# Kernel optimization log

Hardware: AMD Instinct MI355X
Metric: run time of the kernel (lower is better)

Reference implementation:

```python
import jax, jax.numpy as jnp
import numpy as np

B = 32; N = 512; SEQ_LEN = 8
L = 0.05; T_REF = 5.0; V_TH = 20.0; V_RES = 0.0
SQL = float(np.sqrt(L))
BN_EPS = 1e-5

# ---- Dawson-style lookup tables for the LIF moment activation (built once, float64) ----
_XG = np.linspace(-10.0, 4.0, 7001)
_DX = _XG[1] - _XG[0]

def _cumtrapz(y):
    return np.concatenate([[0.0], np.cumsum(0.5 * (y[1:] + y[:-1]) * _DX)])

_phi = np.exp(-_XG ** 2)
_I = np.exp(-100.0) / 20.0 + _cumtrapz(_phi)          # int_{-inf}^x e^{-t^2} dt (asymptotic tail at -10)
_g = np.exp(_XG ** 2) * _I                             # 1st Dawson-like function g(x)
_G = _cumtrapz(_g)                                     # int g dx (rel. to -10)
_h = np.exp(_XG ** 2) * _cumtrapz(_phi * _g ** 2)      # 2nd Dawson-like function h(x)
_H = _cumtrapz(_h)                                     # int h dx

XG = jnp.asarray(_XG, jnp.float32)
GT = jnp.asarray(_g, jnp.float32)
GI = jnp.asarray(_G, jnp.float32)
HI = jnp.asarray(_H, jnp.float32)

def _interp(x, tab):
    return jnp.interp(x, XG, tab)

def moment_activate(u, s, rho):
    # Mnn_Activate_Mean / Std / Corr: LIF moment activation
    s = jnp.maximum(s, 1e-6)
    ub = jnp.clip((V_TH * L - u) / (s * SQL), -10.0, 4.0)
    lb = jnp.clip((V_RES * L - u) / (s * SQL), -10.0, 4.0)
    dG = _interp(ub, GI) - _interp(lb, GI)
    ua = 1.0 / (T_REF + (2.0 / L) * dG)                               # mean firing rate
    dH = jnp.maximum(_interp(ub, HI) - _interp(lb, HI), 0.0)
    sa = jnp.sqrt((8.0 / L ** 2) * dH * ua ** 3)                      # firing std
    dg = _interp(ub, GT) - _interp(lb, GT)
    chi = ua ** 2 * (2.0 / L) * dg / (SQL * jnp.maximum(sa, 1e-9))    # linear response coeff
    eye = jnp.eye(rho.shape[-1], dtype=rho.dtype)
    rho_out = chi[:, :, None] * chi[:, None, :] * rho                 # [B,N,N]
    rho_out = rho_out * (1.0 - eye) + eye                             # unit diagonal
    return ua, sa, rho_out

def linear_corr(W, b, u, s, rho):
    # Mnn_Linear_Corr: mean via affine map, covariance via W C W^T
    u_out = u @ W.T + b
    Cin = rho * s[:, :, None] * s[:, None, :]                         # [B,N,N] covariance
    C = jnp.einsum('bik,lk->bil', jnp.einsum('ij,bjk->bik', W, Cin), W)
    var = jnp.clip(jnp.diagonal(C, axis1=1, axis2=2), 0.0, None)
    s_out = jnp.sqrt(var)
    denom = s_out[:, :, None] * s_out[:, None, :]
    rho_out = jnp.where(denom > 1e-12, C / jnp.maximum(denom, 1e-12), 0.0)
    return u_out, s_out, rho_out

def mexi_hat(n, k=0.3):
    dx = 2.0 * np.pi / n
    x = np.arange(0.0, 2.0 * np.pi, dx)[:n]
    y = np.exp(2.0 * (np.cos(x) - 1.0)) * np.cos(2.0 * x)
    j = np.arange(n)
    idx = (j[None, :] - j[:, None]) % n                               # w[i,:] = y.roll(i)
    return y[idx].astype(np.float32)

def setup_inputs() -> dict:
    ks = jax.random.split(jax.random.key(0), 10)
    u = jax.random.normal(ks[0], (B, N), jnp.float32)
    s = jax.random.uniform(ks[1], (B, N), jnp.float32, 0.1, 1.0)
    A = jax.random.normal(ks[2], (B, N, N), jnp.float32) / np.sqrt(N)
    sym = 0.5 * (A + jnp.swapaxes(A, 1, 2))
    eye = jnp.eye(N, dtype=jnp.float32)
    rho = jnp.clip(sym, -0.5, 0.5) * (1.0 - eye) + eye                # valid-ish corr matrix
    u_ext = jax.random.normal(ks[3], (B, N), jnp.float32)
    s_ext = jax.random.uniform(ks[4], (B, N), jnp.float32, 0.1, 1.0)
    W = 0.02 * jax.random.normal(ks[5], (N, N), jnp.float32) + 0.1 * jnp.asarray(mexi_hat(N))
    b = 0.02 * jax.random.normal(ks[6], (N,), jnp.float32)
    W_ext = 0.02 * jax.random.normal(ks[7], (N, N), jnp.float32)
    b_ext = 0.02 * jax.random.normal(ks[8], (N,), jnp.float32)
    w_mean = 2.5 * jnp.ones((N,), jnp.float32)
    b_mean = 2.5 * jnp.ones((N,), jnp.float32)
    w_mean_ext = 2.5 * jnp.ones((N,), jnp.float32)
    b_mean_ext = 2.5 * jnp.ones((N,), jnp.float32)
    return {'u': u, 's': s, 'rho': rho, 'u_ext': u_ext, 's_ext': s_ext,
            'W': W, 'b': b, 'W_ext': W_ext, 'b_ext': b_ext,
            'w_mean': w_mean, 'b_mean': b_mean,
            'w_mean_ext': w_mean_ext, 'b_mean_ext': b_mean_ext,
            'seq_len': SEQ_LEN}

def reference(u, s, rho, u_ext, s_ext, W, b, W_ext, b_ext,
              w_mean, b_mean, w_mean_ext, b_mean_ext, seq_len):
    # external pathway (Mnn_Linear_without_Corr + BN), computed once
    u_e = u_ext @ W_ext.T + b_ext
    s_e = jnp.sqrt((s_ext ** 2) @ (W_ext ** 2).T)
    mean_e = jnp.mean(u_e, axis=0); var_e = jnp.var(u_e, axis=0)
    f_e = w_mean_ext / jnp.sqrt(var_e + BN_EPS)
    s_e = s_e * jnp.abs(f_e)                                          # Mnn_Std_Bn1d (uses pre-BN stats)
    u_e = (u_e - mean_e) * f_e + b_mean_ext

    def step(carry, _):
        u, s, rho = carry
        u, s, rho = linear_corr(W, b, u, s, rho)
        mean = jnp.mean(u, axis=0); var = jnp.var(u, axis=0)
        f = w_mean / jnp.sqrt(var + BN_EPS)
        s = s * jnp.abs(f)
        u = (u - mean) * f + b_mean
        u = u + u_e
        s = jnp.sqrt(s * s + s_e * s_e)
        return moment_activate(u, s, rho), None

    (u, s, rho), _ = jax.lax.scan(step, (u, s, rho), None, length=seq_len)
    return u, s, rho
```

## Files before the change

### kernel.cpp

```cpp
#include <hip/hip_runtime.h>
#include <math.h>


#define BB 32
#define NN 512
#define SEQ 8
#define TG 7001
#define SVN (BB * NN)
#define BUFW 24576

typedef float f32x4 __attribute__((ext_vector_type(4)));
typedef short s16x8 __attribute__((ext_vector_type(8)));

__device__ __forceinline__ unsigned short bf16_rne(float v) {
    unsigned u = __float_as_uint(v);
    u += 0x7FFFu + ((u >> 16) & 1u);
    return (unsigned short)(u >> 16);
}
__device__ __forceinline__ float bf16_f(unsigned short h) {
    return __uint_as_float(((unsigned)h) << 16);
}
__device__ __forceinline__ void split2(float v, unsigned short& h, unsigned short& l) {
    unsigned short hh = bf16_rne(v);
    h = hh;
    l = bf16_rne(v - bf16_f(hh));
}

__device__ __forceinline__ size_t ts_idx(int r, int k) {
    return (size_t)(((r >> 4) * 16 + (k >> 5)) * 512 + ((k >> 3) & 3) * 128 + (r & 15) * 8 + (k & 7));
}

__device__ __forceinline__ float interp_tab(const float* __restrict__ tab, float x) {
    float t = (x + 10.0f) * 500.0f;
    t = fminf(fmaxf(t, 0.0f), 7000.0f);
    int i0 = (int)t;
    if (i0 > 6999) i0 = 6999;
    float fr = t - (float)i0;
    float a = tab[i0];
    float b = tab[i0 + 1];
    return fmaf(fr, b - a, a);
}

#define GLOAD_LDS16(GP, LP)                                                        \
    __builtin_amdgcn_global_load_lds(                                              \
        (const __attribute__((address_space(1))) unsigned int*)(const void*)(GP),  \
        (__attribute__((address_space(3))) unsigned int*)(void*)(LP), 16, 0, 0)

__global__ void k_exp(double* __restrict__ expP, double* __restrict__ expM) {
    int k = blockIdx.x * 256 + threadIdx.x;
    if (k >= TG) return;
    double x = -10.0 + (14.0 / 7000.0) * k;
    expP[k] = exp(x * x);
    expM[k] = exp(-x * x);
}

__device__ double blk_exscan(double part, double* wsum) {
    int t = threadIdx.x, lane = t & 63, wid = t >> 6;
    double run = part;
    #pragma unroll
    for (int off = 1; off < 64; off <<= 1) {
        double nv = __shfl_up(run, off);
        if (lane >= off) run += nv;
    }
    if (lane == 63) wsum[wid] = run;
    __syncthreads();
    if (t < 16) {
        double v = wsum[t];
        #pragma unroll
        for (int off = 1; off < 16; off <<= 1) {
            double nv = __shfl_up(v, off);
            if (lane >= off) v += nv;
        }
        wsum[t] = v;
    }
    __syncthreads();
    double base = (wid > 0) ? wsum[wid - 1] : 0.0;
    double ex = base + run - part;
    __syncthreads();
    return ex;
}

__global__ __launch_bounds__(1024)
void k_scan(const double* __restrict__ expP, const double* __restrict__ expM,
            float* __restrict__ GT, float* __restrict__ GI, float* __restrict__ HI) {
    __shared__ double ys[7008];
    __shared__ double wsum[16];
    const int t = threadIdx.x;
    const double dx = 14.0 / 7000.0;
    int k0 = t * 7, k1 = k0 + 7;
    if (k1 > TG) k1 = TG;
    if (k0 > TG) k0 = TG;
    int kls = (k0 < 1) ? 1 : k0;

    for (int k = k0; k < k1; ++k) ys[k] = expM[k];
    __syncthreads();

    double tmp[7];
    {
        double part = 0.0;
        for (int k = kls; k < k1; ++k) part += 0.5 * (ys[k - 1] + ys[k]) * dx;
        double run = blk_exscan(part, wsum) + exp(-100.0) / 20.0;
        int c = 0;
        for (int k = k0; k < k1; ++k) {
            if (k >= 1) run += 0.5 * (ys[k - 1] + ys[k]) * dx;
            tmp[c] = expP[k] * run;
            GT[k] = (float)tmp[c];
            ++c;
        }
        __syncthreads();
        c = 0;
        for (int k = k0; k < k1; ++k) ys[k] = tmp[c++];
        __syncthreads();
    }
    {
        double part = 0.0;
        for (int k = kls; k < k1; ++k) part += 0.5 * (ys[k - 1] + ys[k]) * dx;
        double run = blk_exscan(part, wsum);
        for (int k = k0; k < k1; ++k) {
            if (k >= 1) run += 0.5 * (ys[k - 1] + ys[k]) * dx;
            GI[k] = (float)run;
        }
        __syncthreads();
    }
    {
        double part = 0.0;
        for (int k = kls; k < k1; ++k) {
            double ya = expM[k - 1] * ys[k - 1] * ys[k - 1];
            double yb = expM[k] * ys[k] * ys[k];
            part += 0.5 * (ya + yb) * dx;
        }
        double run = blk_exscan(part, wsum);
        int c = 0;
        for (int k = k0; k < k1; ++k) {
            if (k >= 1) {
                double ya = expM[k - 1] * ys[k - 1] * ys[k - 1];
                double yb = expM[k] * ys[k] * ys[k];
                run += 0.5 * (ya + yb) * dx;
            }
            tmp[c++] = run;
        }
        __syncthreads();
        c = 0;
        for (int k = k0; k < k1; ++k) ys[k] = tmp[c++];
        __syncthreads();
    }
    {
        double part = 0.0;
        for (int k = kls; k < k1; ++k)
            part += 0.5 * (expP[k - 1] * ys[k - 1] + expP[k] * ys[k]) * dx;
        double run = blk_exscan(part, wsum);
        for (int k = k0; k < k1; ++k) {
            if (k >= 1) run += 0.5 * (expP[k - 1] * ys[k - 1] + expP[k] * ys[k]) * dx;
            HI[k] = (float)run;
        }
    }
}

__global__ void k_splitW(const float* __restrict__ W,
                         unsigned short* __restrict__ Wh, unsigned short* __restrict__ Wl) {
    int t = blockIdx.x * 256 + threadIdx.x;
    int r = t >> 6, c8 = t & 63;
    int k = c8 * 8;
    const float* src = W + (size_t)r * NN + k;
    s16x8 hv, lv;
    #pragma unroll
    for (int q = 0; q < 8; ++q) {
        unsigned short h, l;
        split2(src[q], h, l);
        hv[q] = (short)h; lv[q] = (short)l;
    }
    size_t o = ts_idx(r, k);
    *reinterpret_cast<s16x8*>(Wh + o) = hv;
    *reinterpret_cast<s16x8*>(Wl + o) = lv;
}

__global__ void k_splitQ(const float* __restrict__ rho, const float* __restrict__ s,
                         unsigned short* __restrict__ Qh, unsigned short* __restrict__ Ql) {
    int t = blockIdx.x * 256 + threadIdx.x;
    int b = t >> 15;
    int rem = t & 32767;
    int r = rem >> 6, c8 = rem & 63;
    int k = c8 * 8;
    const float* src = rho + ((size_t)b * NN + r) * NN + k;
    const float* sb = s + b * NN;
    float si = sb[r];
    s16x8 hv, lv;
    #pragma unroll
    for (int q = 0; q < 8; ++q) {
        float v = src[q] * si * sb[k + q];
        unsigned short h, l;
        split2(v, h, l);
        hv[q] = (short)h; lv[q] = (short)l;
    }
    size_t o = (size_t)b * NN * NN + ts_idx(r, k);
    *reinterpret_cast<s16x8*>(Qh + o) = hv;
    *reinterpret_cast<s16x8*>(Ql + o) = lv;
}

#define MFMAF(AH, AL, BH, BL)                                                  \
    {                                                                          \
        _Pragma("unroll") for (int m_ = 0; m_ < 4; ++m_)                       \
            _Pragma("unroll") for (int n_ = 0; n_ < 2; ++n_)                   \
                acc[m_][n_] = __builtin_amdgcn_mfma_f32_16x16x32_bf16(         \
                    AH[m_], BH[n_], acc[m_][n_], 0, 0, 0);                     \
        _Pragma("unroll") for (int m_ = 0; m_ < 4; ++m_)                       \
            _Pragma("unroll") for (int n_ = 0; n_ < 2; ++n_)                   \
                acc[m_][n_] = __builtin_amdgcn_mfma_f32_16x16x32_bf16(         \
                    AL[m_], BH[n_], acc[m_][n_], 0, 0, 0);                     \
        _Pragma("unroll") for (int m_ = 0; m_ < 4; ++m_)                       \
            _Pragma("unroll") for (int n_ = 0; n_ < 2; ++n_)                   \
                acc[m_][n_] = __builtin_amdgcn_mfma_f32_16x16x32_bf16(         \
                    AH[m_], BL[n_], acc[m_][n_], 0, 0, 0);                     \
    }

template <int PHASE>
__global__ __launch_bounds__(1024, 4)
void gemm_ts(const unsigned short* __restrict__ Ah, const unsigned short* __restrict__ Al,
             long aStride,
             const unsigned short* __restrict__ Bh, const unsigned short* __restrict__ Bl,
             long bStride,
             unsigned short* __restrict__ Oh, unsigned short* __restrict__ Ol,
             float* __restrict__ Of,
             const float* __restrict__ Wf, float* __restrict__ sv,
             const float* __restrict__ u_prev, const float* __restrict__ bvec,
             float* __restrict__ u_linT,
             const float* __restrict__ bn_w, const float* __restrict__ bmv,
             const float* __restrict__ u_e, const float* __restrict__ s_e2,
             const float* __restrict__ GT, const float* __restrict__ GI,
             const float* __restrict__ HI,
             float* __restrict__ u_next, float* __restrict__ s_next) {
    __shared__ __align__(16) unsigned short stg[3 * BUFW];
    __shared__ float slS[384], chS[384], snS[384];

    const int id = blockIdx.x;
    const int b = id >> 3;
    const int combo = id & 7;
    const int yt = combo >> 2;
    const int xt = combo & 3;
    const int i0 = yt * 256, j0 = xt * 128;
    const int tid = threadIdx.x;
    const int w = tid >> 6, lane = tid & 63;
    const int wqm = w >> 2, wqn = w & 3;
    const int laneo = lane * 8;

    const int c0 = w * 3;
    const unsigned short* gp[3];
    #pragma unroll
    for (int q = 0; q < 3; ++q) {
        const int c = c0 + q;
        const unsigned short* src;
        if (c < 16)      src = Ah + (size_t)b * aStride + (size_t)((i0 >> 4) + c) * 8192;
        else if (c < 32) src = Al + (size_t)b * aStride + (size_t)((i0 >> 4) + c - 16) * 8192;
        else if (c < 40) src = Bh + (size_t)b * bStride + (size_t)((j0 >> 4) + c - 32) * 8192;
        else             src = Bl + (size_t)b * bStride + (size_t)((j0 >> 4) + c - 40) * 8192;
        gp[q] = src + laneo;
    }
    auto STAGEQ = [&](int buf, int kb) {
        #pragma unroll
        for (int q = 0; q < 3; ++q)
            GLOAD_LDS16(gp[q] + (size_t)kb * 512, stg + buf * BUFW + (c0 + q) * 512);
    };

    STAGEQ(0, 0);

    if (PHASE == 0) {
        const int row = combo * 64 + (tid >> 4);
        const int seg = tid & 15;
        const float4* wr = (const float4*)(Wf + (size_t)row * NN + seg * 32);
        const float4* ur = (const float4*)(u_prev + b * NN + seg * 32);
        float a0 = 0.f, a1 = 0.f, a2 = 0.f, a3 = 0.f;
        #pragma unroll
        for (int kk = 0; kk < 8; ++kk) {
            float4 wv = wr[kk], uv = ur[kk];
            a0 = fmaf(wv.x, uv.x, a0);
            a1 = fmaf(wv.y, uv.y, a1);
            a2 = fmaf(wv.z, uv.z, a2);
            a3 = fmaf(wv.w, uv.w, a3);
        }
        float au = (a0 + a1) + (a2 + a3);
        au += __shfl_xor(au, 1);
        au += __shfl_xor(au, 2);
        au += __shfl_xor(au, 4);
        au += __shfl_xor(au, 8);
        if (seg == 0) u_linT[row * BB + b] = au + bvec[row];
    } else if (tid < 384) {
        const int ii = (tid < 256) ? (i0 + tid) : (j0 + tid - 256);
        float vb[32];
        {
            const float4* ul = (const float4*)(u_linT + (size_t)ii * BB);
            #pragma unroll
            for (int q = 0; q < 8; ++q) {
                float4 t4 = ul[q];
                vb[q * 4 + 0] = t4.x; vb[q * 4 + 1] = t4.y;
                vb[q * 4 + 2] = t4.z; vb[q * 4 + 3] = t4.w;
            }
        }
        float m = 0.0f;
        #pragma unroll
        for (int bb = 0; bb < BB; ++bb) m += vb[bb];
        m *= (1.0f / BB);
        float v = 0.0f;
        #pragma unroll
        for (int bb = 0; bb < BB; ++bb) {
            float d = vb[bb] - m;
            v = fmaf(d, d, v);
        }
        v *= (1.0f / BB);
        float f = bn_w[ii] / sqrtf(v + 1e-5f);
        const int idx = b * NN + ii;
        float s2;
        {
            const float* svp = sv + idx;
            float q0 = (svp[0 * SVN] + svp[1 * SVN]) + (svp[2 * SVN] + svp[3 * SVN]);
            float q1 = (svp[4 * SVN] + svp[5 * SVN]) + (svp[6 * SVN] + svp[7 * SVN]);
            float q2 = (svp[8 * SVN] + svp[9 * SVN]) + (svp[10 * SVN] + svp[11 * SVN]);
            float q3 = (svp[12 * SVN] + svp[13 * SVN]) + (svp[14 * SVN] + svp[15 * SVN]);
            s2 = (q0 + q1) + (q2 + q3);
        }
        float s_l = sqrtf(fmaxf(s2, 0.0f));
        float un = fmaf(vb[b] - m, f, bmv[ii]) + u_e[idx];
        float sn = sqrtf(fmaf((s_l * s_l) * f, f, s_e2[idx]));
        const float SQL = 0.22360679774997896f;
        float ss = fmaxf(sn, 1e-6f);
        float inv = 1.0f / (ss * SQL);
        float ubx = fminf(fmaxf((1.0f - un) * inv, -10.0f), 4.0f);
        float lbx = fminf(fmaxf((0.0f - un) * inv, -10.0f), 4.0f);
        float dG = interp_tab(GI, ubx) - interp_tab(GI, lbx);
        float ua = 1.0f / fmaf(40.0f, dG, 5.0f);
        float dH = fmaxf(interp_tab(HI, ubx) - interp_tab(HI, lbx), 0.0f);
        float sa = sqrtf(3200.0f * dH * ua * ua * ua);
        float dg2 = interp_tab(GT, ubx) - interp_tab(GT, lbx);
        float ch = ua * ua * 40.0f * dg2 / (SQL * fmaxf(sa, 1e-9f));
        slS[tid] = s_l;
        chS[tid] = ch;
        snS[tid] = sa;
        if (yt == 0 && tid >= 256) {
            u_next[idx] = ua;
            s_next[idx] = sa;
        }
    }

    f32x4 acc[4][2];
    #pragma unroll
    for (int m2 = 0; m2 < 4; ++m2)
        #pragma unroll
        for (int n2 = 0; n2 < 2; ++n2) acc[m2][n2] = (f32x4){0.f, 0.f, 0.f, 0.f};

    STAGEQ(1, 1);
    asm volatile("s_waitcnt vmcnt(3)" ::: "memory");
    __builtin_amdgcn_sched_barrier(0);
    __builtin_amdgcn_s_barrier();
    __builtin_amdgcn_sched_barrier(0);

    #pragma unroll
    for (int kb = 0; kb < 16; ++kb) {
        const int cur = kb % 3;
        if (kb < 14) STAGEQ((kb + 2) % 3, kb + 2);
        const unsigned short* lbuf = stg + cur * BUFW;
        s16x8 fah[4], fal[4], fbh[2], fbl[2];
        #pragma unroll
        for (int t = 0; t < 4; ++t) {
            fah[t] = *reinterpret_cast<const s16x8*>(lbuf + (wqm * 4 + t) * 512 + laneo);
            fal[t] = *reinterpret_cast<const s16x8*>(lbuf + (16 + wqm * 4 + t) * 512 + laneo);
        }
        #pragma unroll
        for (int t = 0; t < 2; ++t) {
            fbh[t] = *reinterpret_cast<const s16x8*>(lbuf + (32 + wqn * 2 + t) * 512 + laneo);
            fbl[t] = *reinterpret_cast<const s16x8*>(lbuf + (40 + wqn * 2 + t) * 512 + laneo);
        }
        MFMAF(fah, fal, fbh, fbl);
        if (kb < 14) {
            asm volatile("s_waitcnt vmcnt(3)" ::: "memory");
        } else if (kb == 14) {
            asm volatile("s_waitcnt vmcnt(0)" ::: "memory");
        }
        __builtin_amdgcn_sched_barrier(0);
        __builtin_amdgcn_s_barrier();
        __builtin_amdgcn_sched_barrier(0);
    }

    const size_t bofs = (size_t)b * NN * NN;
    const int rb0 = i0 + wqm * 64 + (lane >> 4) * 4;
    const int cb0 = j0 + wqn * 32 + (lane & 15);

    if (PHASE == 0) {
        float dp[16];
        #pragma unroll
        for (int m2 = 0; m2 < 4; ++m2)
            #pragma unroll
            for (int r = 0; r < 4; ++r) {
                int row = rb0 + m2 * 16 + r;
                const float* wrow = Wf + ((size_t)row << 9) + cb0;
                float s = 0.0f;
                #pragma unroll
                for (int n2 = 0; n2 < 2; ++n2) s = fmaf(acc[m2][n2][r], wrow[n2 * 16], s);
                dp[m2 * 4 + r] = s;
            }
        #pragma unroll
        for (int k = 0; k < 16; ++k) {
            #pragma unroll
            for (int off = 1; off < 16; off <<= 1) dp[k] += __shfl_xor(dp[k], off);
        }
        if ((lane & 15) == 0) {
            float* svslot = sv + (size_t)(xt * 4 + wqn) * SVN + b * NN;
            #pragma unroll
            for (int k = 0; k < 16; ++k) {
                int row = rb0 + (k >> 2) * 16 + (k & 3);
                svslot[row] = dp[k];
            }
        }
    }

    if (PHASE == 2) {
        float* fS = (float*)stg + w * 2048;
        #pragma unroll
        for (int m2 = 0; m2 < 4; ++m2)
            #pragma unroll
            for (int r = 0; r < 4; ++r) {
                const int lr = m2 * 16 + (lane >> 4) * 4 + r;
                const float si = slS[wqm * 64 + lr], ci = chS[wqm * 64 + lr];
                const int row = i0 + wqm * 64 + lr;
                #pragma unroll
                for (int n2 = 0; n2 < 2; ++n2) {
                    const int lc = wqn * 32 + n2 * 16 + (lane & 15);
                    const float sj = slS[256 + lc], cj = chS[256 + lc];
                    const int col = j0 + lc;
                    float denom = si * sj;
                    float rv = (denom > 1e-12f) ? (acc[m2][n2][r] / fmaxf(denom, 1e-12f)) : 0.0f;
                    rv *= ci * cj;
                    if (row == col) rv = 1.0f;
                    fS[lr * 32 + n2 * 16 + (lane & 15)] = rv;
                }
            }
        #pragma unroll
        for (int inst = 0; inst < 8; ++inst) {
            const int row = i0 + wqm * 64 + inst * 8 + (lane >> 3);
            const int col = j0 + wqn * 32 + (lane & 7) * 4;
            *reinterpret_cast<f32x4*>(Of + bofs + ((size_t)row << 9) + col) =
                *reinterpret_cast<const f32x4*>(fS + inst * 256 + (lane >> 3) * 32 + (lane & 7) * 4);
        }
    } else {
        unsigned short* hiS = stg + w * 4096;
        unsigned short* loS = hiS + 2048;
        const int laneconst = (((lane & 15) >> 3) << 7) + ((lane >> 4) << 5) + (lane & 7);
        #pragma unroll
        for (int m2 = 0; m2 < 4; ++m2)
            #pragma unroll
            for (int n2 = 0; n2 < 2; ++n2) {
                const int base = laneconst + m2 * 512 + n2 * 256;
                #pragma unroll
                for (int r = 0; r < 4; ++r) {
                    float v;
                    if (PHASE == 0) {
                        v = acc[m2][n2][r];
                    } else {
                        const int lr = wqm * 64 + m2 * 16 + (lane >> 4) * 4 + r;
                        const int lc = wqn * 32 + n2 * 16 + (lane & 15);
                        const float si = slS[lr], ci = chS[lr], qi = snS[lr];
                        const float sj = slS[256 + lc], cj = chS[256 + lc], qj = snS[256 + lc];
                        float denom = si * sj;
                        float rv = (denom > 1e-12f) ? (acc[m2][n2][r] / fmaxf(denom, 1e-12f)) : 0.0f;
                        rv *= ci * cj;
                        if (i0 + lr == j0 + lc) rv = 1.0f;
                        v = rv * qi * qj;
                    }
                    unsigned short h, l;
                    split2(v, h, l);
                    hiS[base + r * 8] = h;
                    loS[base + r * 8] = l;
                }
            }
        #pragma unroll
        for (int lb_ = 0; lb_ < 4; ++lb_) {
            const int gb = ((i0 >> 4) + wqm * 4 + lb_) * 16 + (j0 >> 5) + wqn;
            *reinterpret_cast<s16x8*>(Oh + bofs + (size_t)gb * 512 + laneo) =
                *reinterpret_cast<const s16x8*>(hiS + lb_ * 512 + laneo);
            *reinterpret_cast<s16x8*>(Ol + bofs + (size_t)gb * 512 + laneo) =
                *reinterpret_cast<const s16x8*>(loS + lb_ * 512 + laneo);
        }
    }
}

__global__ void k_ext_dots(const float* __restrict__ Wx, const float* __restrict__ bx,
                           const float* __restrict__ ux, const float* __restrict__ sx,
                           float* __restrict__ u_e, float* __restrict__ s_e2) {
    int gw = (blockIdx.x << 2) + (threadIdx.x >> 6);
    int lane = threadIdx.x & 63;
    int b = gw >> 9, i = gw & 511;
    const float* wr = Wx + (size_t)i * NN;
    const float* ub = ux + b * NN;
    const float* sb = sx + b * NN;
    float au = 0.0f, as2 = 0.0f;
    for (int j = lane; j < NN; j += 64) {
        float w = wr[j];
        float s = sb[j];
        au = fmaf(w, ub[j], au);
        as2 = fmaf(w * w, s * s, as2);
    }
    #pragma unroll
    for (int off = 32; off; off >>= 1) {
        au += __shfl_down(au, off);
        as2 += __shfl_down(as2, off);
    }
    if (lane == 0) {
        u_e[b * NN + i] = au + bx[i];
        s_e2[b * NN + i] = as2;
    }
}

__global__ void k_ext_stats(float* __restrict__ u_e, float* __restrict__ s_e2,
                            const float* __restrict__ wmx, const float* __restrict__ bmx) {
    int i = blockIdx.x * blockDim.x + threadIdx.x;
    if (i >= NN) return;
    float m = 0.0f;
    for (int b = 0; b < BB; ++b) m += u_e[b * NN + i];
    m *= (1.0f / BB);
    float v = 0.0f;
    for (int b = 0; b < BB; ++b) {
        float d = u_e[b * NN + i] - m;
        v = fmaf(d, d, v);
    }
    v *= (1.0f / BB);
    float f = wmx[i] / sqrtf(v + 1e-5f);
    float bm = bmx[i];
    for (int b = 0; b < BB; ++b) {
        u_e[b * NN + i] = fmaf(u_e[b * NN + i] - m, f, bm);
        s_e2[b * NN + i] *= f * f;
    }
}

extern "C" void kernel_launch(void* const* d_in, const int* in_sizes, int n_in,
                              void* d_out, int out_size, void* d_ws, size_t ws_size,
                              hipStream_t stream) {
    (void)in_sizes; (void)n_in; (void)out_size; (void)ws_size;
    const float* u_in       = (const float*)d_in[0];
    const float* s_in       = (const float*)d_in[1];
    const float* rho_in     = (const float*)d_in[2];
    const float* u_ext      = (const float*)d_in[3];
    const float* s_ext      = (const float*)d_in[4];
    const float* W          = (const float*)d_in[5];
    const float* bvec       = (const float*)d_in[6];
    const float* W_ext      = (const float*)d_in[7];
    const float* b_ext      = (const float*)d_in[8];
    const float* w_mean     = (const float*)d_in[9];
    const float* b_mean     = (const float*)d_in[10];
    const float* w_mean_ext = (const float*)d_in[11];
    const float* b_mean_ext = (const float*)d_in[12];

    float* out_u   = (float*)d_out;
    float* out_s   = out_u + BB * NN;
    float* out_rho = out_s + BB * NN;
    unsigned short* Qh = (unsigned short*)out_rho;
    unsigned short* Ql = Qh + (size_t)BB * NN * NN;

    char* base = (char*)d_ws;
    size_t off = 0;
    auto alloc = [&](size_t bytes) -> char* {
        char* ptr = base + off;
        off += (bytes + 255) & ~(size_t)255;
        return ptr;
    };
    unsigned short* T1h = (unsigned short*)alloc((size_t)BB * NN * NN * 2);
    unsigned short* T1l = (unsigned short*)alloc((size_t)BB * NN * NN * 2);
    unsigned short* Wh  = (unsigned short*)alloc((size_t)NN * NN * 2);
    unsigned short* Wl  = (unsigned short*)alloc((size_t)NN * NN * 2);
    double* expP = (double*)alloc(TG * 8);
    double* expM = (double*)alloc(TG * 8);
    float* GTt   = (float*)alloc(TG * 4);
    float* GIt   = (float*)alloc(TG * 4);
    float* HIt   = (float*)alloc(TG * 4);
    float* u_e   = (float*)alloc(BB * NN * 4);
    float* s_e2  = (float*)alloc(BB * NN * 4);
    float* uA    = (float*)alloc(BB * NN * 4);
    float* uB2   = (float*)alloc(BB * NN * 4);
    float* sA    = (float*)alloc(BB * NN * 4);
    float* sB2   = (float*)alloc(BB * NN * 4);
    float* u_linT = (float*)alloc(BB * NN * 4);
    float* sv    = (float*)alloc((size_t)16 * BB * NN * 4);

    k_exp<<<28, 256, 0, stream>>>(expP, expM);
    k_scan<<<1, 1024, 0, stream>>>(expP, expM, GTt, GIt, HIt);
    k_splitW<<<128, 256, 0, stream>>>(W, Wh, Wl);
    k_splitQ<<<4096, 256, 0, stream>>>(rho_in, s_in, Qh, Ql);
    k_ext_dots<<<BB * NN / 4, 256, 0, stream>>>(W_ext, b_ext, u_ext, s_ext, u_e, s_e2);
    k_ext_stats<<<2, 256, 0, stream>>>(u_e, s_e2, w_mean_ext, b_mean_ext);

    const float* cu = u_in;

    for (int t = 0; t < SEQ; ++t) {
        gemm_ts<0><<<256, 1024, 0, stream>>>(
            Wh, Wl, 0L, Qh, Ql, (long)NN * NN, T1h, T1l, nullptr,
            W, sv, cu, bvec, u_linT,
            nullptr, nullptr, nullptr, nullptr, nullptr, nullptr, nullptr,
            nullptr, nullptr);
        float* nu = (t == SEQ - 1) ? out_u : ((t & 1) ? uA : uB2);
        float* ns = (t == SEQ - 1) ? out_s : ((t & 1) ? sA : sB2);
        if (t < SEQ - 1) {
            gemm_ts<1><<<256, 1024, 0, stream>>>(
                T1h, T1l, (long)NN * NN, Wh, Wl, 0L, Qh, Ql, nullptr,
                nullptr, sv, nullptr, nullptr, u_linT,
                w_mean, b_mean, u_e, s_e2, GTt, GIt, HIt, nu, ns);
        } else {
            gemm_ts<2><<<256, 1024, 0, stream>>>(
                T1h, T1l, (long)NN * NN, Wh, Wl, 0L, nullptr, nullptr, out_rho,
                nullptr, sv, nullptr, nullptr, u_linT,
                w_mean, b_mean, u_e, s_e2, GTt, GIt, HIt, nu, ns);
        }
        cu = nu;
    }
}
```

Before: 787.5 us.

## Shrink GEMM block tile to 128x64 with 512 threads and 4x more blocks

Halves the output tile per block from 256x128 to 128x64 with 8 waves instead of 16, so the grid grows from 256 to 1024 blocks. The LDS staging buffers, per-wave accumulators and epilogue indexing shrink to match, and the second prefetch stage is issued earlier. This is meant to fill the 256 CUs better and allow more blocks per CU. In exchange, each smaller tile reuses its operands less, so more global traffic is spent re-reading the A and B panels.

```diff
diff --git a/kernel.cpp b/kernel.cpp
--- a/kernel.cpp
+++ b/kernel.cpp
@@ -7,7 +7,7 @@
 #define SEQ 8
 #define TG 7001
 #define SVN (BB * NN)
-#define BUFW 24576
+#define BUFW 12288
 
 typedef float f32x4 __attribute__((ext_vector_type(4)));
 typedef short s16x8 __attribute__((ext_vector_type(8)));
@@ -199,22 +199,29 @@
 
 #define MFMAF(AH, AL, BH, BL)                                                  \
     {                                                                          \
-        _Pragma("unroll") for (int m_ = 0; m_ < 4; ++m_)                       \
+        _Pragma("unroll") for (int m_ = 0; m_ < 2; ++m_)                       \
             _Pragma("unroll") for (int n_ = 0; n_ < 2; ++n_)                   \
                 acc[m_][n_] = __builtin_amdgcn_mfma_f32_16x16x32_bf16(         \
                     AH[m_], BH[n_], acc[m_][n_], 0, 0, 0);                     \
-        _Pragma("unroll") for (int m_ = 0; m_ < 4; ++m_)                       \
+        _Pragma("unroll") for (int m_ = 0; m_ < 2; ++m_)                       \
             _Pragma("unroll") for (int n_ = 0; n_ < 2; ++n_)                   \
                 acc[m_][n_] = __builtin_amdgcn_mfma_f32_16x16x32_bf16(         \
                     AL[m_], BH[n_], acc[m_][n_], 0, 0, 0);                     \
-        _Pragma("unroll") for (int m_ = 0; m_ < 4; ++m_)                       \
+        _Pragma("unroll") for (int m_ = 0; m_ < 2; ++m_)                       \
             _Pragma("unroll") for (int n_ = 0; n_ < 2; ++n_)                   \
                 acc[m_][n_] = __builtin_amdgcn_mfma_f32_16x16x32_bf16(         \
                     AH[m_], BL[n_], acc[m_][n_], 0, 0, 0);                     \
     }
 
+#define STAGE(BUF, KB)                                                         \
+    {                                                                          \
+        _Pragma("unroll") for (int q_ = 0; q_ < 3; ++q_)                       \
+            GLOAD_LDS16(gp[q_] + (size_t)(KB) * 512,                           \
+                        stg + (BUF) * BUFW + (c0 + q_) * 512);                 \
+    }
+
 template <int PHASE>
-__global__ __launch_bounds__(1024, 4)
+__global__ __launch_bounds__(512, 4)
 void gemm_ts(const unsigned short* __restrict__ Ah, const unsigned short* __restrict__ Al,
              long aStride,
              const unsigned short* __restrict__ Bh, const unsigned short* __restrict__ Bl,
@@ -230,17 +237,17 @@
              const float* __restrict__ HI,
              float* __restrict__ u_next, float* __restrict__ s_next) {
     __shared__ __align__(16) unsigned short stg[3 * BUFW];
-    __shared__ float slS[384], chS[384], snS[384];
+    __shared__ float slS[192], chS[192], snS[192];
 
     const int id = blockIdx.x;
-    const int b = id >> 3;
-    const int combo = id & 7;
-    const int yt = combo >> 2;
-    const int xt = combo & 3;
-    const int i0 = yt * 256, j0 = xt * 128;
+    const int b = id >> 5;
+    const int tile = id & 31;
+    const int yt = tile >> 3;
+    const int xt = tile & 7;
+    const int i0 = yt * 128, j0 = xt * 64;
     const int tid = threadIdx.x;
     const int w = tid >> 6, lane = tid & 63;
-    const int wqm = w >> 2, wqn = w & 3;
+    const int wqm = w >> 1, wqn = w & 1;
     const int laneo = lane * 8;
 
     const int c0 = w * 3;
@@ -249,42 +256,40 @@
     for (int q = 0; q < 3; ++q) {
         const int c = c0 + q;
         const unsigned short* src;
-        if (c < 16)      src = Ah + (size_t)b * aStride + (size_t)((i0 >> 4) + c) * 8192;
-        else if (c < 32) src = Al + (size_t)b * aStride + (size_t)((i0 >> 4) + c - 16) * 8192;
-        else if (c < 40) src = Bh + (size_t)b * bStride + (size_t)((j0 >> 4) + c - 32) * 8192;
-        else             src = Bl + (size_t)b * bStride + (size_t)((j0 >> 4) + c - 40) * 8192;
+        if (c < 8)       src = Ah + (size_t)b * aStride + (size_t)((i0 >> 4) + c) * 8192;
+        else if (c < 16) src = Al + (size_t)b * aStride + (size_t)((i0 >> 4) + c - 8) * 8192;
+        else if (c < 20) src = Bh + (size_t)b * bStride + (size_t)((j0 >> 4) + c - 16) * 8192;
+        else             src = Bl + (size_t)b * bStride + (size_t)((j0 >> 4) + c - 20) * 8192;
         gp[q] = src + laneo;
     }
-    auto STAGEQ = [&](int buf, int kb) {
-        #pragma unroll
-        for (int q = 0; q < 3; ++q)
-            GLOAD_LDS16(gp[q] + (size_t)kb * 512, stg + buf * BUFW + (c0 + q) * 512);
-    };
-
-    STAGEQ(0, 0);
+
+    STAGE(0, 0);
+    STAGE(1, 1);
 
     if (PHASE == 0) {
-        const int row = combo * 64 + (tid >> 4);
-        const int seg = tid & 15;
-        const float4* wr = (const float4*)(Wf + (size_t)row * NN + seg * 32);
-        const float4* ur = (const float4*)(u_prev + b * NN + seg * 32);
-        float a0 = 0.f, a1 = 0.f, a2 = 0.f, a3 = 0.f;
-        #pragma unroll
-        for (int kk = 0; kk < 8; ++kk) {
-            float4 wv = wr[kk], uv = ur[kk];
-            a0 = fmaf(wv.x, uv.x, a0);
-            a1 = fmaf(wv.y, uv.y, a1);
-            a2 = fmaf(wv.z, uv.z, a2);
-            a3 = fmaf(wv.w, uv.w, a3);
-        }
-        float au = (a0 + a1) + (a2 + a3);
-        au += __shfl_xor(au, 1);
-        au += __shfl_xor(au, 2);
-        au += __shfl_xor(au, 4);
-        au += __shfl_xor(au, 8);
-        if (seg == 0) u_linT[row * BB + b] = au + bvec[row];
-    } else if (tid < 384) {
-        const int ii = (tid < 256) ? (i0 + tid) : (j0 + tid - 256);
+        if (tid < 256) {
+            const int row = tile * 16 + (tid >> 4);
+            const int seg = tid & 15;
+            const float4* wr = (const float4*)(Wf + (size_t)row * NN + seg * 32);
+            const float4* ur = (const float4*)(u_prev + b * NN + seg * 32);
+            float a0 = 0.f, a1 = 0.f, a2 = 0.f, a3 = 0.f;
+            #pragma unroll
+            for (int kk = 0; kk < 8; ++kk) {
+                float4 wv = wr[kk], uv = ur[kk];
+                a0 = fmaf(wv.x, uv.x, a0);
+                a1 = fmaf(wv.y, uv.y, a1);
+                a2 = fmaf(wv.z, uv.z, a2);
+                a3 = fmaf(wv.w, uv.w, a3);
+            }
+            float au = (a0 + a1) + (a2 + a3);
+            au += __shfl_xor(au, 1);
+            au += __shfl_xor(au, 2);
+            au += __shfl_xor(au, 4);
+            au += __shfl_xor(au, 8);
+            if (seg == 0) u_linT[row * BB + b] = au + bvec[row];
+        }
+    } else if (tid < 192) {
+        const int ii = (tid < 128) ? (i0 + tid) : (j0 + tid - 128);
         float vb[32];
         {
             const float4* ul = (const float4*)(u_linT + (size_t)ii * BB);
@@ -334,19 +339,18 @@
         slS[tid] = s_l;
         chS[tid] = ch;
         snS[tid] = sa;
-        if (yt == 0 && tid >= 256) {
+        if (yt == 0 && tid >= 128) {
             u_next[idx] = ua;
             s_next[idx] = sa;
         }
     }
 
-    f32x4 acc[4][2];
+    f32x4 acc[2][2];
     #pragma unroll
-    for (int m2 = 0; m2 < 4; ++m2)
+    for (int m2 = 0; m2 < 2; ++m2)
         #pragma unroll
         for (int n2 = 0; n2 < 2; ++n2) acc[m2][n2] = (f32x4){0.f, 0.f, 0.f, 0.f};
 
-    STAGEQ(1, 1);
     asm volatile("s_waitcnt vmcnt(3)" ::: "memory");
     __builtin_amdgcn_sched_barrier(0);
     __builtin_amdgcn_s_barrier();
@@ -355,18 +359,15 @@
     #pragma unroll
     for (int kb = 0; kb < 16; ++kb) {
         const int cur = kb % 3;
-        if (kb < 14) STAGEQ((kb + 2) % 3, kb + 2);
+        if (kb < 14) STAGE((kb + 2) % 3, kb + 2);
         const unsigned short* lbuf = stg + cur * BUFW;
-        s16x8 fah[4], fal[4], fbh[2], fbl[2];
-        #pragma unroll
-        for (int t = 0; t < 4; ++t) {
-            fah[t] = *reinterpret_cast<const s16x8*>(lbuf + (wqm * 4 + t) * 512 + laneo);
-            fal[t] = *reinterpret_cast<const s16x8*>(lbuf + (16 + wqm * 4 + t) * 512 + laneo);
-        }
+        s16x8 fah[2], fal[2], fbh[2], fbl[2];
         #pragma unroll
         for (int t = 0; t < 2; ++t) {
-            fbh[t] = *reinterpret_cast<const s16x8*>(lbuf + (32 + wqn * 2 + t) * 512 + laneo);
-            fbl[t] = *reinterpret_cast<const s16x8*>(lbuf + (40 + wqn * 2 + t) * 512 + laneo);
+            fah[t] = *reinterpret_cast<const s16x8*>(lbuf + (wqm * 2 + t) * 512 + laneo);
+            fal[t] = *reinterpret_cast<const s16x8*>(lbuf + (8 + wqm * 2 + t) * 512 + laneo);
+            fbh[t] = *reinterpret_cast<const s16x8*>(lbuf + (16 + wqn * 2 + t) * 512 + laneo);
+            fbl[t] = *reinterpret_cast<const s16x8*>(lbuf + (20 + wqn * 2 + t) * 512 + laneo);
         }
         MFMAF(fah, fal, fbh, fbl);
         if (kb < 14) {
@@ -380,13 +381,13 @@
     }
 
     const size_t bofs = (size_t)b * NN * NN;
-    const int rb0 = i0 + wqm * 64 + (lane >> 4) * 4;
+    const int rb0 = i0 + wqm * 32 + (lane >> 4) * 4;
     const int cb0 = j0 + wqn * 32 + (lane & 15);
 
     if (PHASE == 0) {
-        float dp[16];
-        #pragma unroll
-        for (int m2 = 0; m2 < 4; ++m2)
+        float dp[8];
+        #pragma unroll
+        for (int m2 = 0; m2 < 2; ++m2)
             #pragma unroll
             for (int r = 0; r < 4; ++r) {
                 int row = rb0 + m2 * 16 + r;
@@ -397,14 +398,14 @@
                 dp[m2 * 4 + r] = s;
             }
         #pragma unroll
-        for (int k = 0; k < 16; ++k) {
+        for (int k = 0; k < 8; ++k) {
             #pragma unroll
             for (int off = 1; off < 16; off <<= 1) dp[k] += __shfl_xor(dp[k], off);
         }
         if ((lane & 15) == 0) {
-            float* svslot = sv + (size_t)(xt * 4 + wqn) * SVN + b * NN;
+            float* svslot = sv + (size_t)(xt * 2 + wqn) * SVN + b * NN;
             #pragma unroll
-            for (int k = 0; k < 16; ++k) {
+            for (int k = 0; k < 8; ++k) {
                 int row = rb0 + (k >> 2) * 16 + (k & 3);
                 svslot[row] = dp[k];
             }
@@ -412,18 +413,18 @@
     }
 
     if (PHASE == 2) {
-        float* fS = (float*)stg + w * 2048;
-        #pragma unroll
-        for (int m2 = 0; m2 < 4; ++m2)
+        float* fS = (float*)stg + w * 1024;
+        #pragma unroll
+        for (int m2 = 0; m2 < 2; ++m2)
             #pragma unroll
             for (int r = 0; r < 4; ++r) {
                 const int lr = m2 * 16 + (lane >> 4) * 4 + r;
-                const float si = slS[wqm * 64 + lr], ci = chS[wqm * 64 + lr];
-                const int row = i0 + wqm * 64 + lr;
+                const float si = slS[wqm * 32 + lr], ci = chS[wqm * 32 + lr];
+                const int row = i0 + wqm * 32 + lr;
                 #pragma unroll
                 for (int n2 = 0; n2 < 2; ++n2) {
                     const int lc = wqn * 32 + n2 * 16 + (lane & 15);
-                    const float sj = slS[256 + lc], cj = chS[256 + lc];
+                    const float sj = slS[128 + lc], cj = chS[128 + lc];
                     const int col = j0 + lc;
                     float denom = si * sj;
                     float rv = (denom > 1e-12f) ? (acc[m2][n2][r] / fmaxf(denom, 1e-12f)) : 0.0f;
@@ -433,18 +434,18 @@
                 }
             }
         #pragma unroll
-        for (int inst = 0; inst < 8; ++inst) {
-            const int row = i0 + wqm * 64 + inst * 8 + (lane >> 3);
+        for (int inst = 0; inst < 4; ++inst) {
+            const int row = i0 + wqm * 32 + inst * 8 + (lane >> 3);
             const int col = j0 + wqn * 32 + (lane & 7) * 4;
             *reinterpret_cast<f32x4*>(Of + bofs + ((size_t)row << 9) + col) =
                 *reinterpret_cast<const f32x4*>(fS + inst * 256 + (lane >> 3) * 32 + (lane & 7) * 4);
         }
     } else {
-        unsigned short* hiS = stg + w * 4096;
-        unsigned short* loS = hiS + 2048;
+        unsigned short* hiS = stg + w * 2048;
+        unsigned short* loS = hiS + 1024;
         const int laneconst = (((lane & 15) >> 3) << 7) + ((lane >> 4) << 5) + (lane & 7);
         #pragma unroll
-        for (int m2 = 0; m2 < 4; ++m2)
+        for (int m2 = 0; m2 < 2; ++m2)
             #pragma unroll
             for (int n2 = 0; n2 < 2; ++n2) {
                 const int base = laneconst + m2 * 512 + n2 * 256;
@@ -454,10 +455,10 @@
                     if (PHASE == 0) {
                         v = acc[m2][n2][r];
                     } else {
-                        const int lr = wqm * 64 + m2 * 16 + (lane >> 4) * 4 + r;
+                        const int lr = wqm * 32 + m2 * 16 + (lane >> 4) * 4 + r;
                         const int lc = wqn * 32 + n2 * 16 + (lane & 15);
                         const float si = slS[lr], ci = chS[lr], qi = snS[lr];
-                        const float sj = slS[256 + lc], cj = chS[256 + lc], qj = snS[256 + lc];
+                        const float sj = slS[128 + lc], cj = chS[128 + lc], qj = snS[128 + lc];
                         float denom = si * sj;
                         float rv = (denom > 1e-12f) ? (acc[m2][n2][r] / fmaxf(denom, 1e-12f)) : 0.0f;
                         rv *= ci * cj;
@@ -471,12 +472,12 @@
                 }
             }
         #pragma unroll
-        for (int lb_ = 0; lb_ < 4; ++lb_) {
-            const int gb = ((i0 >> 4) + wqm * 4 + lb_) * 16 + (j0 >> 5) + wqn;
+        for (int t2 = 0; t2 < 2; ++t2) {
+            const int gb = ((i0 >> 4) + wqm * 2 + t2) * 16 + (j0 >> 5) + wqn;
             *reinterpret_cast<s16x8*>(Oh + bofs + (size_t)gb * 512 + laneo) =
-                *reinterpret_cast<const s16x8*>(hiS + lb_ * 512 + laneo);
+                *reinterpret_cast<const s16x8*>(hiS + t2 * 512 + laneo);
             *reinterpret_cast<s16x8*>(Ol + bofs + (size_t)gb * 512 + laneo) =
-                *reinterpret_cast<const s16x8*>(loS + lb_ * 512 + laneo);
+                *reinterpret_cast<const s16x8*>(loS + t2 * 512 + laneo);
         }
     }
 }
@@ -588,7 +589,7 @@
     const float* cu = u_in;
 
     for (int t = 0; t < SEQ; ++t) {
-        gemm_ts<0><<<256, 1024, 0, stream>>>(
+        gemm_ts<0><<<1024, 512, 0, stream>>>(
             Wh, Wl, 0L, Qh, Ql, (long)NN * NN, T1h, T1l, nullptr,
             W, sv, cu, bvec, u_linT,
             nullptr, nullptr, nullptr, nullptr, nullptr, nullptr, nullptr,
@@ -596,12 +597,12 @@
         float* nu = (t == SEQ - 1) ? out_u : ((t & 1) ? uA : uB2);
         float* ns = (t == SEQ - 1) ? out_s : ((t & 1) ? sA : sB2);
         if (t < SEQ - 1) {
-            gemm_ts<1><<<256, 1024, 0, stream>>>(
+            gemm_ts<1><<<1024, 512, 0, stream>>>(
                 T1h, T1l, (long)NN * NN, Wh, Wl, 0L, Qh, Ql, nullptr,
                 nullptr, sv, nullptr, nullptr, u_linT,
                 w_mean, b_mean, u_e, s_e2, GTt, GIt, HIt, nu, ns);
         } else {
-            gemm_ts<2><<<256, 1024, 0, stream>>>(
+            gemm_ts<2><<<1024, 512, 0, stream>>>(
                 T1h, T1l, (long)NN * NN, Wh, Wl, 0L, nullptr, nullptr, out_rho,
                 nullptr, sv, nullptr, nullptr, u_linT,
                 w_mean, b_mean, u_e, s_e2, GTt, GIt, HIt, nu, ns);
```

After: 870.9 us. 1.11x slower.
